# Kernel tuning notes

Hardware: AMD Instinct MI355X
Metric: run time of the kernel (lower is better)

## Reference

```python
import jax, jax.numpy as jnp
import numpy as np

N, D, E = 16384, 1024, 8

def setup_inputs() -> dict:
    key = jax.random.key(0)
    ks = jax.random.split(key, 5)
    s = 1.0 / np.sqrt(D)
    return {
        "x": jax.random.normal(ks[0], (N, D), dtype=jnp.float32),
        "router_w": jax.random.uniform(ks[1], (E, D), jnp.float32, -s, s),   # torch Linear weight [out,in]
        "router_b": jax.random.uniform(ks[2], (E,), jnp.float32, -s, s),
        "expert_w": jax.random.uniform(ks[3], (E, D, D), jnp.float32, -s, s),  # [E, out, in]
        "expert_b": jax.random.uniform(ks[4], (E, D), jnp.float32, -s, s),
    }

def reference(x, router_w, router_b, expert_w, expert_b):
    # Router: logits -> softmax -> argmax (argmax of softmax == argmax of logits)
    logits = x @ router_w.T + router_b            # [N, E]
    top = jnp.argmax(logits, axis=-1)             # [N]
    # Compute all expert outputs (vectorized grouped GEMM), then select top-1.
    # Faithful to the torch loop: output is the raw expert output, NOT gate-scaled.
    xe = jnp.einsum('nd,eod->neo', x, expert_w) + expert_b[None, :, :]  # [N, E, D]
    out = jnp.take_along_axis(xe, top[:, None, None], axis=1)[:, 0, :]  # [N, D]
    return out
```

## Files before the change

### kernel.cpp

```cpp
#include <hip/hip_runtime.h>
#include <hip/hip_bf16.h>


#define NTOK 16384
#define DIM  1024
#define NEXP 8

#define AS1 __attribute__((address_space(1)))
#define AS3 __attribute__((address_space(3)))

typedef __bf16 bf16x8 __attribute__((ext_vector_type(8)));
typedef float  f32x4  __attribute__((ext_vector_type(4)));

__device__ __forceinline__ unsigned int f2bf(float f) {
  unsigned int u = __builtin_bit_cast(unsigned int, f);
  u += 0x7FFFu + ((u >> 16) & 1u);
  return u >> 16;
}

__global__ __launch_bounds__(256) void k_router(const float* __restrict__ x,
                                                const float* __restrict__ rw,
                                                const float* __restrict__ rb,
                                                const float* __restrict__ ew,
                                                unsigned short* __restrict__ xbf,
                                                unsigned short* __restrict__ wbf,
                                                int* __restrict__ top) {
  __shared__ float wlds[NEXP * DIM];
  const int tid = threadIdx.x;

  if (blockIdx.x & 1) {
    const int cb = blockIdx.x >> 1;
#pragma unroll
    for (int pass = 0; pass < 4; ++pass) {
      size_t i = ((size_t)(pass * 1024 + cb) * 256 + tid) * 8;
      const float4* p = (const float4*)(ew + i);
      float4 a = p[0], b = p[1];
      unsigned int w0 = f2bf(a.x) | (f2bf(a.y) << 16);
      unsigned int w1 = f2bf(a.z) | (f2bf(a.w) << 16);
      unsigned int w2 = f2bf(b.x) | (f2bf(b.y) << 16);
      unsigned int w3 = f2bf(b.z) | (f2bf(b.w) << 16);
      *(uint4*)(wbf + i) = make_uint4(w0, w1, w2, w3);
    }
    return;
  }

  const int rbid = blockIdx.x >> 1;
  const int lane = tid & 63;
  const int wave = tid >> 6;
#pragma unroll
  for (int i = 0; i < 8; ++i)
    ((float4*)wlds)[tid + 256 * i] = ((const float4*)rw)[tid + 256 * i];
  __syncthreads();

  const int ea = lane & 7;
  const float bias = rb[ea];

#pragma unroll 1
  for (int tp = 0; tp < 2; ++tp) {
    const int nA = (rbid << 4) + (wave << 2) + (tp << 1);
    const int nB = nA + 1;

    float4 xa[4], xb[4];
#pragma unroll
    for (int j = 0; j < 4; ++j) {
      xa[j] = *(const float4*)(x + ((size_t)nA << 10) + (j << 8) + (lane << 2));
      xb[j] = *(const float4*)(x + ((size_t)nB << 10) + (j << 8) + (lane << 2));
    }

#pragma unroll
    for (int j = 0; j < 4; ++j) {
      uint2 sa, sb;
      sa.x = f2bf(xa[j].x) | (f2bf(xa[j].y) << 16);
      sa.y = f2bf(xa[j].z) | (f2bf(xa[j].w) << 16);
      sb.x = f2bf(xb[j].x) | (f2bf(xb[j].y) << 16);
      sb.y = f2bf(xb[j].z) | (f2bf(xb[j].w) << 16);
      *(uint2*)(xbf + ((size_t)nA << 10) + (j << 8) + (lane << 2)) = sa;
      *(uint2*)(xbf + ((size_t)nB << 10) + (j << 8) + (lane << 2)) = sb;
    }

    double pA[8] = {}, pB[8] = {};
#pragma unroll
    for (int j = 0; j < 4; ++j) {
#pragma unroll
      for (int e = 0; e < 8; ++e) {
        float4 wv = *(const float4*)&wlds[e * 1024 + (j << 8) + (lane << 2)];
        pA[e] += (double)xa[j].x * (double)wv.x;
        pA[e] += (double)xa[j].y * (double)wv.y;
        pA[e] += (double)xa[j].z * (double)wv.z;
        pA[e] += (double)xa[j].w * (double)wv.w;
        pB[e] += (double)xb[j].x * (double)wv.x;
        pB[e] += (double)xb[j].y * (double)wv.y;
        pB[e] += (double)xb[j].z * (double)wv.z;
        pB[e] += (double)xb[j].w * (double)wv.w;
      }
      __builtin_amdgcn_sched_barrier(0);
    }

    float qA[8], qB[8];
#pragma unroll
    for (int e = 0; e < 8; ++e) { qA[e] = (float)pA[e]; qB[e] = (float)pB[e]; }
#pragma unroll
    for (int e = 0; e < 8; ++e) {
      qA[e] += __shfl_xor(qA[e], 1);
      qB[e] += __shfl_xor(qB[e], 1);
      qA[e] += __shfl_xor(qA[e], 2);
      qB[e] += __shfl_xor(qB[e], 2);
      qA[e] += __shfl_xor(qA[e], 4);
      qB[e] += __shfl_xor(qB[e], 4);
    }
    float sA, sB;
    {
      float q0 = (ea & 1) ? qA[1] : qA[0], q1 = (ea & 1) ? qA[3] : qA[2];
      float q2 = (ea & 1) ? qA[5] : qA[4], q3 = (ea & 1) ? qA[7] : qA[6];
      float r0 = (ea & 2) ? q1 : q0, r1 = (ea & 2) ? q3 : q2;
      sA = (ea & 4) ? r1 : r0;
      q0 = (ea & 1) ? qB[1] : qB[0]; q1 = (ea & 1) ? qB[3] : qB[2];
      q2 = (ea & 1) ? qB[5] : qB[4]; q3 = (ea & 1) ? qB[7] : qB[6];
      r0 = (ea & 2) ? q1 : q0; r1 = (ea & 2) ? q3 : q2;
      sB = (ea & 4) ? r1 : r0;
    }
    sA += __shfl_xor(sA, 8);  sB += __shfl_xor(sB, 8);
    sA += __shfl_xor(sA, 16); sB += __shfl_xor(sB, 16);
    sA += __shfl_xor(sA, 32); sB += __shfl_xor(sB, 32);
    sA += bias; sB += bias;
    float bvA = sA, bvB = sB;
    int biA = ea, biB = ea;
#pragma unroll
    for (int mask = 1; mask <= 4; mask <<= 1) {
      float ovA = __shfl_xor(bvA, mask), ovB = __shfl_xor(bvB, mask);
      int oiA = __shfl_xor(biA, mask), oiB = __shfl_xor(biB, mask);
      if (ovA > bvA || (ovA == bvA && oiA < biA)) { bvA = ovA; biA = oiA; }
      if (ovB > bvB || (ovB == bvB && oiB < biB)) { bvB = ovB; biB = oiB; }
    }
    if (lane == 0) {
      top[nA] = biA;
      top[nB] = biB;
    }
  }
}

__global__ __launch_bounds__(1024) void k_sort(const int* __restrict__ top,
                                               int* __restrict__ counts,
                                               int* __restrict__ tok) {
  __shared__ unsigned long long wsum[2][16];
  const int t = threadIdx.x;
  const int lane = t & 63;
  const int wv = t >> 6;

  int4 v[4];
  const int4* tp = (const int4*)(top + t * 16);
#pragma unroll
  for (int i = 0; i < 4; ++i) v[i] = tp[i];

  unsigned long long h0 = 0, h1 = 0;
#pragma unroll
  for (int i = 0; i < 16; ++i) {
    int e = ((const int*)v)[i];
    if (e < 4) h0 += 1ull << (16 * e);
    else       h1 += 1ull << (16 * (e - 4));
  }

  unsigned long long s0 = h0, s1 = h1;
#pragma unroll
  for (int d = 1; d < 64; d <<= 1) {
    unsigned long long t0 = __shfl_up(s0, d);
    unsigned long long t1 = __shfl_up(s1, d);
    if (lane >= d) { s0 += t0; s1 += t1; }
  }
  if (lane == 63) { wsum[0][wv] = s0; wsum[1][wv] = s1; }
  __syncthreads();

  unsigned long long base0 = 0, base1 = 0;
#pragma unroll
  for (int i = 0; i < 15; ++i) {
    if (i < wv) { base0 += wsum[0][i]; base1 += wsum[1][i]; }
  }
  unsigned long long b0 = base0 + s0 - h0;
  unsigned long long b1 = base1 + s1 - h1;

  if (t == 1023) {
    unsigned long long i0 = base0 + s0, i1 = base1 + s1;
#pragma unroll
    for (int e = 0; e < 4; ++e) counts[e] = (int)((i0 >> (16 * e)) & 0xFFFF);
#pragma unroll
    for (int e = 0; e < 4; ++e) counts[4 + e] = (int)((i1 >> (16 * e)) & 0xFFFF);
  }

#pragma unroll
  for (int i = 0; i < 16; ++i) {
    int e = ((const int*)v)[i];
    int pos;
    if (e < 4) {
      pos = (int)((b0 >> (16 * e)) & 0xFFFF);
      b0 += 1ull << (16 * e);
    } else {
      int f = e - 4;
      pos = (int)((b1 >> (16 * f)) & 0xFFFF);
      b1 += 1ull << (16 * f);
    }
    tok[(e << 14) + pos] = t * 16 + i;
  }
}

__global__ __launch_bounds__(256, 2) void k_gemm(const unsigned short* __restrict__ xbf,
                                                 const unsigned short* __restrict__ wbf,
                                                 const float* __restrict__ eb,
                                                 const int* __restrict__ counts,
                                                 const int* __restrict__ tokall,
                                                 float* __restrict__ out) {
  const int bid = blockIdx.x;
  const int e = bid & 7;
  const int loc = bid >> 3;
  const int cb = loc & 7;
  const int t = loc >> 3;
  const int c = counts[e];
  if (t * 128 >= c) return;
  const int n0 = cb << 7;
  const int* tok = tokall + (e << 14);
  const int tid = threadIdx.x;
  const int lane = tid & 63;
  const int wave = tid >> 6;

  __shared__ unsigned short As[2][128 * 64];
  __shared__ unsigned short Bs[2][128 * 64];

  const int prow = tid >> 3;
  const int pchk = tid & 7;
  size_t asrc[4], bsrc[4];
  const unsigned short* wb = wbf + ((size_t)e << 20);
#pragma unroll
  for (int s = 0; s < 4; ++s) {
    int row = s * 32 + prow;
    int m = t * 128 + row;
    int g = tok[(m < c) ? m : 0];
    int l = pchk ^ (row & 7);
    asrc[s] = (size_t)g * DIM + (size_t)l * 8;
    bsrc[s] = (size_t)(n0 + row) * DIM + (size_t)l * 8;
  }

  f32x4 acc[4][4] = {};
  const int wr = wave >> 1, wc = wave & 1;

  int aoff[2][4], boff[2][4];
#pragma unroll
  for (int h = 0; h < 2; ++h)
#pragma unroll
    for (int m = 0; m < 4; ++m) {
      int row = wr * 64 + m * 16 + (lane & 15);
      int p = (h * 4 + (lane >> 4)) ^ (row & 7);
      aoff[h][m] = row * 64 + p * 8;
      int rowb = wc * 64 + m * 16 + (lane & 15);
      int pb = (h * 4 + (lane >> 4)) ^ (rowb & 7);
      boff[h][m] = rowb * 64 + pb * 8;
    }

  auto stage = [&](int b, int k0) {
#pragma unroll
    for (int s = 0; s < 4; ++s) {
      __builtin_amdgcn_global_load_lds(
          (const AS1 unsigned int*)(xbf + asrc[s] + k0),
          (AS3 unsigned int*)(&As[b][s * 2048 + wave * 512]),
          16, 0, 0);
      __builtin_amdgcn_global_load_lds(
          (const AS1 unsigned int*)(wb + bsrc[s] + k0),
          (AS3 unsigned int*)(&Bs[b][s * 2048 + wave * 512]),
          16, 0, 0);
    }
  };

  stage(0, 0);
  for (int k = 0; k < 16; ++k) {
    if (k < 15) {
      stage((k + 1) & 1, (k + 1) * 64);
      asm volatile("s_waitcnt vmcnt(8)" ::: "memory");
    } else {
      asm volatile("s_waitcnt vmcnt(0)" ::: "memory");
    }
    __builtin_amdgcn_s_barrier();
    __builtin_amdgcn_sched_barrier(0);
    const unsigned short* Ab = As[k & 1];
    const unsigned short* Bb = Bs[k & 1];
#pragma unroll
    for (int h = 0; h < 2; ++h) {
      bf16x8 af[4], bfr[4];
#pragma unroll
      for (int m = 0; m < 4; ++m) af[m] = *(const bf16x8*)&Ab[aoff[h][m]];
#pragma unroll
      for (int n = 0; n < 4; ++n) bfr[n] = *(const bf16x8*)&Bb[boff[h][n]];
#pragma unroll
      for (int m = 0; m < 4; ++m)
#pragma unroll
        for (int n = 0; n < 4; ++n)
          acc[m][n] = __builtin_amdgcn_mfma_f32_16x16x32_bf16(af[m], bfr[n], acc[m][n], 0, 0, 0);
    }
    __builtin_amdgcn_s_barrier();
  }

  const int colb = n0 + wc * 64 + (lane & 15);
  float bias[4];
#pragma unroll
  for (int n = 0; n < 4; ++n) bias[n] = eb[(e << 10) + colb + n * 16];
#pragma unroll
  for (int m = 0; m < 4; ++m) {
    int rbase = t * 128 + wr * 64 + m * 16 + ((lane >> 4) << 2);
#pragma unroll
    for (int r = 0; r < 4; ++r) {
      int mm = rbase + r;
      if (mm < c) {
        int g = tok[mm];
        float* op = out + ((size_t)g << 10);
#pragma unroll
        for (int n = 0; n < 4; ++n) op[colb + n * 16] = acc[m][n][r] + bias[n];
      }
    }
  }
}

extern "C" void kernel_launch(void* const* d_in, const int* in_sizes, int n_in,
                              void* d_out, int out_size, void* d_ws, size_t ws_size,
                              hipStream_t stream) {
  const float* x  = (const float*)d_in[0];
  const float* rw = (const float*)d_in[1];
  const float* rb = (const float*)d_in[2];
  const float* ew = (const float*)d_in[3];
  const float* eb = (const float*)d_in[4];
  float* out = (float*)d_out;

  char* ws = (char*)d_ws;
  unsigned short* wbf = (unsigned short*)ws;
  unsigned short* xbf = (unsigned short*)(ws + (16u << 20));
  int* tok    = (int*)(ws + (48u << 20));
  int* counts = (int*)(ws + (48u << 20) + (1u << 19));
  int* top    = (int*)(ws + (48u << 20) + (1u << 19) + 128);

  k_router<<<2048, 256, 0, stream>>>(x, rw, rb, ew, xbf, wbf, top);
  k_sort<<<1, 1024, 0, stream>>>(top, counts, tok);
  k_gemm<<<8192, 256, 0, stream>>>(xbf, wbf, eb, counts, tok, out);
}
```

Measured before the change: 108.0 us.

## Move expert weight conversion into sort kernel and use 8-wave GEMM blocks

Expert-weight fp32-to-bf16 conversion moves from the router kernel into extra blocks of the single-block sort kernel, so it overlaps the serial sort instead of sharing the router launch. The GEMM goes from 4 waves to 8 waves per 128x128 tile, each wave computing 64x32, which halves per-thread staging loads and accumulators. This is meant to raise occupancy and latency hiding, at the cost of more waves contending for the same LDS tile and barrier.

After: 92.66 us (median of 2 runs). 14.2% less time.

```diff
diff --git a/kernel.cpp b/kernel.cpp
--- a/kernel.cpp
+++ b/kernel.cpp
@@ -21,30 +21,10 @@
 __global__ __launch_bounds__(256) void k_router(const float* __restrict__ x,
                                                 const float* __restrict__ rw,
                                                 const float* __restrict__ rb,
-                                                const float* __restrict__ ew,
                                                 unsigned short* __restrict__ xbf,
-                                                unsigned short* __restrict__ wbf,
                                                 int* __restrict__ top) {
   __shared__ float wlds[NEXP * DIM];
   const int tid = threadIdx.x;
-
-  if (blockIdx.x & 1) {
-    const int cb = blockIdx.x >> 1;
-#pragma unroll
-    for (int pass = 0; pass < 4; ++pass) {
-      size_t i = ((size_t)(pass * 1024 + cb) * 256 + tid) * 8;
-      const float4* p = (const float4*)(ew + i);
-      float4 a = p[0], b = p[1];
-      unsigned int w0 = f2bf(a.x) | (f2bf(a.y) << 16);
-      unsigned int w1 = f2bf(a.z) | (f2bf(a.w) << 16);
-      unsigned int w2 = f2bf(b.x) | (f2bf(b.y) << 16);
-      unsigned int w3 = f2bf(b.z) | (f2bf(b.w) << 16);
-      *(uint4*)(wbf + i) = make_uint4(w0, w1, w2, w3);
-    }
-    return;
-  }
-
-  const int rbid = blockIdx.x >> 1;
   const int lane = tid & 63;
   const int wave = tid >> 6;
 #pragma unroll
@@ -57,7 +37,7 @@
 
 #pragma unroll 1
   for (int tp = 0; tp < 2; ++tp) {
-    const int nA = (rbid << 4) + (wave << 2) + (tp << 1);
+    const int nA = (blockIdx.x << 4) + (wave << 2) + (tp << 1);
     const int nB = nA + 1;
 
     float4 xa[4], xb[4];
@@ -139,11 +119,25 @@
   }
 }
 
-__global__ __launch_bounds__(1024) void k_sort(const int* __restrict__ top,
-                                               int* __restrict__ counts,
-                                               int* __restrict__ tok) {
+__global__ __launch_bounds__(1024) void k_sortconv(const float* __restrict__ ew,
+                                                   unsigned short* __restrict__ wbf,
+                                                   const int* __restrict__ top,
+                                                   int* __restrict__ counts,
+                                                   int* __restrict__ tok) {
+  const int t = threadIdx.x;
+  if (blockIdx.x > 0) {
+    size_t i = ((size_t)(blockIdx.x - 1) * 1024 + t) * 8;
+    const float4* p = (const float4*)(ew + i);
+    float4 a = p[0], b = p[1];
+    unsigned int w0 = f2bf(a.x) | (f2bf(a.y) << 16);
+    unsigned int w1 = f2bf(a.z) | (f2bf(a.w) << 16);
+    unsigned int w2 = f2bf(b.x) | (f2bf(b.y) << 16);
+    unsigned int w3 = f2bf(b.z) | (f2bf(b.w) << 16);
+    *(uint4*)(wbf + i) = make_uint4(w0, w1, w2, w3);
+    return;
+  }
+
   __shared__ unsigned long long wsum[2][16];
-  const int t = threadIdx.x;
   const int lane = t & 63;
   const int wv = t >> 6;
 
@@ -185,7 +179,6 @@
 #pragma unroll
     for (int e = 0; e < 4; ++e) counts[4 + e] = (int)((i1 >> (16 * e)) & 0xFFFF);
   }
-
 #pragma unroll
   for (int i = 0; i < 16; ++i) {
     int e = ((const int*)v)[i];
@@ -202,7 +195,7 @@
   }
 }
 
-__global__ __launch_bounds__(256, 2) void k_gemm(const unsigned short* __restrict__ xbf,
+__global__ __launch_bounds__(512, 2) void k_gemm(const unsigned short* __restrict__ xbf,
                                                  const unsigned short* __restrict__ wbf,
                                                  const float* __restrict__ eb,
                                                  const int* __restrict__ counts,
@@ -219,18 +212,20 @@
   const int* tok = tokall + (e << 14);
   const int tid = threadIdx.x;
   const int lane = tid & 63;
-  const int wave = tid >> 6;
+  const int w = tid >> 6;
+  const int wr = w >> 2;
+  const int wn = w & 3;
 
   __shared__ unsigned short As[2][128 * 64];
   __shared__ unsigned short Bs[2][128 * 64];
 
   const int prow = tid >> 3;
   const int pchk = tid & 7;
-  size_t asrc[4], bsrc[4];
+  size_t asrc[2], bsrc[2];
   const unsigned short* wb = wbf + ((size_t)e << 20);
 #pragma unroll
-  for (int s = 0; s < 4; ++s) {
-    int row = s * 32 + prow;
+  for (int s = 0; s < 2; ++s) {
+    int row = s * 64 + prow;
     int m = t * 128 + row;
     int g = tok[(m < c) ? m : 0];
     int l = pchk ^ (row & 7);
@@ -238,32 +233,35 @@
     bsrc[s] = (size_t)(n0 + row) * DIM + (size_t)l * 8;
   }
 
-  f32x4 acc[4][4] = {};
-  const int wr = wave >> 1, wc = wave & 1;
-
-  int aoff[2][4], boff[2][4];
-#pragma unroll
-  for (int h = 0; h < 2; ++h)
+  f32x4 acc[4][2] = {};
+
+  int aoff[2][4], boff[2][2];
+#pragma unroll
+  for (int h = 0; h < 2; ++h) {
 #pragma unroll
     for (int m = 0; m < 4; ++m) {
       int row = wr * 64 + m * 16 + (lane & 15);
       int p = (h * 4 + (lane >> 4)) ^ (row & 7);
       aoff[h][m] = row * 64 + p * 8;
-      int rowb = wc * 64 + m * 16 + (lane & 15);
+    }
+#pragma unroll
+    for (int n = 0; n < 2; ++n) {
+      int rowb = wn * 32 + n * 16 + (lane & 15);
       int pb = (h * 4 + (lane >> 4)) ^ (rowb & 7);
-      boff[h][m] = rowb * 64 + pb * 8;
-    }
+      boff[h][n] = rowb * 64 + pb * 8;
+    }
+  }
 
   auto stage = [&](int b, int k0) {
 #pragma unroll
-    for (int s = 0; s < 4; ++s) {
+    for (int s = 0; s < 2; ++s) {
       __builtin_amdgcn_global_load_lds(
           (const AS1 unsigned int*)(xbf + asrc[s] + k0),
-          (AS3 unsigned int*)(&As[b][s * 2048 + wave * 512]),
+          (AS3 unsigned int*)(&As[b][s * 4096 + w * 512]),
           16, 0, 0);
       __builtin_amdgcn_global_load_lds(
           (const AS1 unsigned int*)(wb + bsrc[s] + k0),
-          (AS3 unsigned int*)(&Bs[b][s * 2048 + wave * 512]),
+          (AS3 unsigned int*)(&Bs[b][s * 4096 + w * 512]),
           16, 0, 0);
     }
   };
@@ -272,7 +270,7 @@
   for (int k = 0; k < 16; ++k) {
     if (k < 15) {
       stage((k + 1) & 1, (k + 1) * 64);
-      asm volatile("s_waitcnt vmcnt(8)" ::: "memory");
+      asm volatile("s_waitcnt vmcnt(4)" ::: "memory");
     } else {
       asm volatile("s_waitcnt vmcnt(0)" ::: "memory");
     }
@@ -282,24 +280,24 @@
     const unsigned short* Bb = Bs[k & 1];
 #pragma unroll
     for (int h = 0; h < 2; ++h) {
-      bf16x8 af[4], bfr[4];
+      bf16x8 af[4], bfr[2];
 #pragma unroll
       for (int m = 0; m < 4; ++m) af[m] = *(const bf16x8*)&Ab[aoff[h][m]];
 #pragma unroll
-      for (int n = 0; n < 4; ++n) bfr[n] = *(const bf16x8*)&Bb[boff[h][n]];
+      for (int n = 0; n < 2; ++n) bfr[n] = *(const bf16x8*)&Bb[boff[h][n]];
 #pragma unroll
       for (int m = 0; m < 4; ++m)
 #pragma unroll
-        for (int n = 0; n < 4; ++n)
+        for (int n = 0; n < 2; ++n)
           acc[m][n] = __builtin_amdgcn_mfma_f32_16x16x32_bf16(af[m], bfr[n], acc[m][n], 0, 0, 0);
     }
     __builtin_amdgcn_s_barrier();
   }
 
-  const int colb = n0 + wc * 64 + (lane & 15);
-  float bias[4];
-#pragma unroll
-  for (int n = 0; n < 4; ++n) bias[n] = eb[(e << 10) + colb + n * 16];
+  const int colb = n0 + wn * 32 + (lane & 15);
+  float bias[2];
+#pragma unroll
+  for (int n = 0; n < 2; ++n) bias[n] = eb[(e << 10) + colb + n * 16];
 #pragma unroll
   for (int m = 0; m < 4; ++m) {
     int rbase = t * 128 + wr * 64 + m * 16 + ((lane >> 4) << 2);
@@ -310,7 +308,7 @@
         int g = tok[mm];
         float* op = out + ((size_t)g << 10);
 #pragma unroll
-        for (int n = 0; n < 4; ++n) op[colb + n * 16] = acc[m][n][r] + bias[n];
+        for (int n = 0; n < 2; ++n) op[colb + n * 16] = acc[m][n][r] + bias[n];
       }
     }
   }
@@ -333,7 +331,7 @@
   int* counts = (int*)(ws + (48u << 20) + (1u << 19));
   int* top    = (int*)(ws + (48u << 20) + (1u << 19) + 128);
 
-  k_router<<<2048, 256, 0, stream>>>(x, rw, rb, ew, xbf, wbf, top);
-  k_sort<<<1, 1024, 0, stream>>>(top, counts, tok);
-  k_gemm<<<8192, 256, 0, stream>>>(xbf, wbf, eb, counts, tok, out);
-}
+  k_router<<<NTOK / 16, 256, 0, stream>>>(x, rw, rb, xbf, top);
+  k_sortconv<<<1025, 1024, 0, stream>>>(ew, wbf, top, counts, tok);
+  k_gemm<<<8192, 512, 0, stream>>>(xbf, wbf, eb, counts, tok, out);
+}
```
